# Optimization experiments

Hardware: AMD Instinct MI355X
Metric: run time of the kernel (lower is better)

The kernel has to match this reference:

```python
import jax, jax.numpy as jnp
from jax import lax
import numpy as np

ITER_ = 10
SMOOTH = 1.0

# ---------- soft skeletonization (clDice-style, 2D) ----------

def _max_pool(x, wh, ww):
    # x: [B,1,H,W]
    return lax.reduce_window(x, -jnp.inf, lax.max, (1, 1, wh, ww), (1, 1, 1, 1), 'SAME')

def _soft_erode(x):
    return jnp.minimum(-_max_pool(-x, 3, 1), -_max_pool(-x, 1, 3))

def _soft_dilate(x):
    return _max_pool(x, 3, 3)

def _soft_open(x):
    return _soft_dilate(_soft_erode(x))

def soft_skel(img, iters):
    skel = jax.nn.relu(img - _soft_open(img))
    for _ in range(iters):
        img = _soft_erode(img)
        delta = jax.nn.relu(img - _soft_open(img))
        skel = skel + jax.nn.relu(delta - skel * delta)
    return skel

# ---------- exact 2D Euclidean distance transform ----------

def _edt2d(mask):
    # mask: [H,W] bool, True = foreground. distance to nearest background pixel.
    H, W = mask.shape
    BIG = jnp.float32(H + W)
    z = ~mask  # background indicator
    def step(d, zr):
        d = jnp.where(zr, 0.0, jnp.minimum(d + 1.0, BIG))
        return d, d
    init = jnp.full((H,), BIG, jnp.float32)
    _, f = lax.scan(step, init, z.T)            # [W,H] forward along rows
    _, b = lax.scan(step, init, z.T[::-1])      # backward
    g = jnp.minimum(f, b[::-1]).T               # [H,W] 1D row distance
    ys = jnp.arange(H, dtype=jnp.float32)
    diff2 = (ys[:, None] - ys[None, :]) ** 2    # [H,H]
    # lower envelope over columns: d2[y,x] = min_y' g[y',x]^2 + (y-y')^2
    d2 = jnp.min(g[None, :, :] ** 2 + diff2[:, :, None], axis=1)  # [H,W]
    return jnp.sqrt(d2)

_edt_batched = jax.vmap(_edt2d)  # [B,H,W] bool -> [B,H,W] float

# ---------- cbDice pieces ----------

def combine_tensors(A, B, C):
    return jnp.where((A != 0) & (B == 0), A * C, B * C)

def get_weights(mask_input, skel_input, prob_flag):
    # mask_input/skel_input: [B,H,W] float
    mask = mask_input > 0.5
    skel = skel_input > 0.5
    dist = lax.stop_gradient(_edt_batched(mask))       # EDT of binary mask, non-diff
    distances = jnp.where(mask, dist, 0.0)
    skel_radius = jnp.where(skel, distances, 0.0)
    rmax = jnp.maximum(jnp.max(skel_radius, axis=(1, 2), keepdims=True), 1.0)
    rmin = jnp.maximum(jnp.min(skel_radius, axis=(1, 2), keepdims=True), 1.0)
    d_clip = jnp.minimum(distances, rmax)
    dist_map_norm = d_clip / rmax
    skel_R_norm = skel_radius / rmax
    I_norm = (rmax - skel_radius + rmin) / rmax        # dim == 2 branch
    I_norm = jnp.where(skel, I_norm, 0.0)
    if prob_flag:
        return dist_map_norm * mask_input, skel_R_norm * mask_input, I_norm * skel_input
    m = mask.astype(jnp.float32)
    s = skel.astype(jnp.float32)
    return dist_map_norm * m, skel_R_norm * m, I_norm * s

def soft_cb_dice_loss(y_pred, y_true):
    p = jax.nn.sigmoid(y_pred)                              # [B,1,H,W]
    pb = jnp.concatenate([1.0 - p, p], axis=1)              # [B,2,H,W]
    pp = jax.nn.softmax(pb, axis=1)[:, 1]                   # [B,H,W]
    yt = jnp.where(y_true > 0, 1.0, 0.0)[:, 0]              # [B,H,W]
    hard = lax.stop_gradient((pp > 0.5).astype(jnp.float32))
    skel_pred_hard = lax.stop_gradient(soft_skel(hard[:, None], ITER_)[:, 0])
    skel_true = lax.stop_gradient(soft_skel(yt[:, None], ITER_)[:, 0])
    skel_pred_prob = skel_pred_hard * pp
    q_vl, q_slvl, q_sl = get_weights(yt, skel_true, False)
    q_vp, q_spvp, q_sp = get_weights(pp, skel_pred_prob, True)
    w_tprec = (jnp.sum(q_sp * q_vl) + SMOOTH) / (jnp.sum(combine_tensors(q_spvp, q_slvl, q_sp)) + SMOOTH)
    w_tsens = (jnp.sum(q_sl * q_vp) + SMOOTH) / (jnp.sum(combine_tensors(q_slvl, q_spvp, q_sl)) + SMOOTH)
    return 1.0 - 2.0 * (w_tprec * w_tsens) / (w_tprec + w_tsens)

def setup_inputs() -> dict:
    key = jax.random.key(0)
    k1, k2 = jax.random.split(key)
    y_pred = jax.random.normal(k1, (4, 1, 256, 256), dtype=jnp.float32)
    y_true = jax.random.randint(k2, (4, 1, 256, 256), 0, 2, dtype=jnp.int32)
    return {"y_pred": y_pred, "y_true": y_true}

def reference(y_pred, y_true):
    return soft_cb_dice_loss(y_pred, y_true)
```

## Files before the change

### kernel.cpp

```cpp
#include <hip/hip_runtime.h>

typedef unsigned long long u64;

#define NIMG 4
#define H 256
#define W 256
#define NPIX (H*W)
#define NTOT (NIMG*NPIX)
#define WPR 4
#define WPI (H*WPR)
#define WPB (NIMG*WPI)
#define XT 16

__global__ void prep_kernel(const float* __restrict__ y_pred,
                            const int* __restrict__ y_true,
                            float* __restrict__ pp,
                            u64* __restrict__ mask_bits,
                            unsigned* __restrict__ rmm_u,
                            double* __restrict__ sums) {
  if (blockIdx.x == 0) {
    if (threadIdx.x < 16) rmm_u[threadIdx.x] = (threadIdx.x & 1) ? 0x7F800000u : 0u;
    else if (threadIdx.x < 20) sums[threadIdx.x - 16] = 0.0;
  }
  int i = blockIdx.x * 256 + threadIdx.x;
  float x = y_pred[i];
  float p = 1.0f / (1.0f + expf(-x));
  float q = 1.0f / (1.0f + expf(-(2.0f * p - 1.0f)));
  pp[i] = q;
  u64 bt = __ballot(y_true[i] > 0);
  u64 bp = __ballot(q > 0.5f);
  if ((threadIdx.x & 63) == 0) {
    mask_bits[i >> 6] = bt;
    mask_bits[WPB + (i >> 6)] = bp;
  }
}

__device__ __forceinline__ void erode_from(const u64 S[][WPR], int y, u64 out[WPR]) {
  u64 c[WPR], up[WPR], dn[WPR];
#pragma unroll
  for (int k = 0; k < WPR; ++k) {
    c[k]  = S[y][k];
    up[k] = (y > 0)     ? S[y-1][k] : ~0ULL;
    dn[k] = (y < H-1)   ? S[y+1][k] : ~0ULL;
  }
#pragma unroll
  for (int k = 0; k < WPR; ++k) {
    u64 l = (c[k] << 1) | ((k > 0)     ? (c[k-1] >> 63) : 1ULL);
    u64 r = (c[k] >> 1) | ((k < WPR-1) ? (c[k+1] << 63) : 0x8000000000000000ULL);
    out[k] = c[k] & up[k] & dn[k] & l & r;
  }
}

__device__ __forceinline__ void dilate_from(const u64 S[][WPR], int y, u64 out[WPR]) {
  u64 v[WPR];
#pragma unroll
  for (int k = 0; k < WPR; ++k) {
    u64 a = S[y][k];
    if (y > 0)   a |= S[y-1][k];
    if (y < H-1) a |= S[y+1][k];
    v[k] = a;
  }
#pragma unroll
  for (int k = 0; k < WPR; ++k) {
    u64 l = (v[k] << 1) | ((k > 0)     ? (v[k-1] >> 63) : 0ULL);
    u64 r = (v[k] >> 1) | ((k < WPR-1) ? (v[k+1] << 63) : 0ULL);
    out[k] = v[k] | l | r;
  }
}

__global__ void skel_kernel(const u64* __restrict__ mask_bits,
                            u64* __restrict__ skel_bits) {
  __shared__ u64 SA[H][WPR];
  __shared__ u64 SB[H][WPR];
  int y = threadIdx.x;
  int base = blockIdx.x * WPI;
  u64 a[WPR], cur[WPR], e[WPR], d[WPR], sk[WPR];
#pragma unroll
  for (int k = 0; k < WPR; ++k) { a[k] = mask_bits[base + y*WPR + k]; SA[y][k] = a[k]; }
  __syncthreads();
  erode_from(SA, y, e);
#pragma unroll
  for (int k = 0; k < WPR; ++k) SB[y][k] = e[k];
  __syncthreads();
  dilate_from(SB, y, d);
#pragma unroll
  for (int k = 0; k < WPR; ++k) { sk[k] = a[k] & ~d[k]; cur[k] = e[k]; }
  u64 (*P)[WPR] = SB;
  u64 (*Q)[WPR] = SA;
  for (int it = 0; it < 10; ++it) {
    erode_from(P, y, e);
#pragma unroll
    for (int k = 0; k < WPR; ++k) Q[y][k] = e[k];
    __syncthreads();
    dilate_from(Q, y, d);
#pragma unroll
    for (int k = 0; k < WPR; ++k) { sk[k] |= cur[k] & ~d[k]; cur[k] = e[k]; }
    u64 (*T)[WPR] = P; P = Q; Q = T;
  }
#pragma unroll
  for (int k = 0; k < WPR; ++k) skel_bits[base + y*WPR + k] = sk[k];
}

__global__ void edt_cols_kernel(const u64* __restrict__ mask_bits,
                                const u64* __restrict__ skel_bits,
                                float* __restrict__ edt,
                                unsigned* __restrict__ rmm_u) {
  __shared__ float col2[H][XT + 1];
  int bi = blockIdx.x >> 4;
  int xt = blockIdx.x & 15;
  int x0 = xt * XT;
  int kx = x0 >> 6;
  int sh0 = x0 & 63;
  int t = threadIdx.x;
  {
    int y = t;
    const u64* row = mask_bits + bi*WPI + y*WPR;
    u64 z[WPR];
#pragma unroll
    for (int k = 0; k < WPR; ++k) z[k] = ~row[k];
#pragma unroll
    for (int xx = 0; xx < XT; ++xx) {
      int x = x0 + xx;
      int bx = x & 63;
      int ld = 512;
      {
        u64 w = z[kx] & ((bx == 63) ? ~0ULL : ((1ULL << (bx+1)) - 1ULL));
        for (int k = kx; ; ) {
          if (w) { int pos = 63 - __builtin_clzll(w) + (k << 6); ld = x - pos; break; }
          if (--k < 0) break;
          w = z[k];
        }
      }
      int rd = 512;
      {
        u64 w = z[kx] & (~0ULL << bx);
        for (int k = kx; ; ) {
          if (w) { int pos = __builtin_ctzll(w) + (k << 6); rd = pos - x; break; }
          if (++k > WPR-1) break;
          w = z[k];
        }
      }
      int g = min(ld, rd);
      col2[y][xx] = (float)(g * g);
    }
  }
  __syncthreads();
  int x  = t & (XT - 1);
  int yg = t >> 4;
  float vmax = 0.0f, vmin = 3.0e38f;
#pragma unroll
  for (int j = 0; j < 16; ++j) {
    int y = yg * 16 + j;
    float best = col2[y][x];
    for (int k = 1; k < H; ++k) {
      float k2 = (float)(k * k);
      if (k2 >= best) break;
      int ym = y - k, yq = y + k;
      if (ym >= 0) best = fminf(best, col2[ym][x] + k2);
      if (yq < H)  best = fminf(best, col2[yq][x] + k2);
    }
    float dist = sqrtf(best);
    edt[bi*NPIX + y*W + x0 + x] = dist;
    u64 sw = skel_bits[bi*WPI + y*WPR + kx];
    int sb = (int)((sw >> (sh0 + x)) & 1ULL);
    float srad = sb ? dist : 0.0f;
    vmax = fmaxf(vmax, srad);
    vmin = fminf(vmin, srad);
  }
  for (int o = 32; o > 0; o >>= 1) {
    vmax = fmaxf(vmax, __shfl_down(vmax, o, 64));
    vmin = fminf(vmin, __shfl_down(vmin, o, 64));
  }
  __shared__ float smax[4], smin[4];
  int wave = t >> 6, lane = t & 63;
  if (lane == 0) { smax[wave] = vmax; smin[wave] = vmin; }
  __syncthreads();
  if (t == 0) {
    float mx = smax[0], mn = smin[0];
    for (int wv = 1; wv < 4; ++wv) { mx = fmaxf(mx, smax[wv]); mn = fminf(mn, smin[wv]); }
    atomicMax(&rmm_u[bi*2 + 0], __float_as_uint(mx));
    atomicMin(&rmm_u[bi*2 + 1], __float_as_uint(mn));
  }
}

__global__ void final_sum_kernel(const float* __restrict__ edt,
                                 const u64* __restrict__ mask_bits,
                                 const u64* __restrict__ skel_bits,
                                 const float* __restrict__ pp,
                                 const unsigned* __restrict__ rmm_u,
                                 double* __restrict__ sums) {
  int i0 = (blockIdx.x * 256 + threadIdx.x) * 4;
  int img = i0 >> 16;
  int wi = i0 >> 6;
  int b0 = i0 & 63;
  u64 mw_t = mask_bits[wi];
  u64 sw_t = skel_bits[wi];
  u64 sw_p = skel_bits[WPB + wi];
  float4 d_t4 = *(const float4*)(edt + i0);
  float4 d_p4 = *(const float4*)(edt + NTOT + i0);
  float4 pp4  = *(const float4*)(pp + i0);
  float rmax_t = fmaxf(__uint_as_float(rmm_u[img*2 + 0]), 1.0f);
  float rmin_t = fmaxf(__uint_as_float(rmm_u[img*2 + 1]), 1.0f);
  float rmax_p = fmaxf(__uint_as_float(rmm_u[(4+img)*2 + 0]), 1.0f);
  float rmin_p = fmaxf(__uint_as_float(rmm_u[(4+img)*2 + 1]), 1.0f);
  float t1 = 0.f, t2 = 0.f, t3 = 0.f, t4 = 0.f;
  float dts[4] = {d_t4.x, d_t4.y, d_t4.z, d_t4.w};
  float dps[4] = {d_p4.x, d_p4.y, d_p4.z, d_p4.w};
  float pps[4] = {pp4.x, pp4.y, pp4.z, pp4.w};
#pragma unroll
  for (int j = 0; j < 4; ++j) {
    int b = b0 + j;
    int m_t = (int)((mw_t >> b) & 1ULL);
    int s_t = (int)((sw_t >> b) & 1ULL);
    float distances_t = m_t ? dts[j] : 0.0f;
    float skelrad_t   = s_t ? distances_t : 0.0f;
    float dmn_t = fminf(distances_t, rmax_t) / rmax_t;
    float srn_t = skelrad_t / rmax_t;
    float In_t  = s_t ? (rmax_t - skelrad_t + rmin_t) / rmax_t : 0.0f;
    float q_vl   = m_t ? dmn_t : 0.0f;
    float q_slvl = m_t ? srn_t : 0.0f;
    float q_sl   = s_t ? In_t  : 0.0f;
    int s_pb = (int)((sw_p >> b) & 1ULL);
    float ppv = pps[j];
    float skel_in_p = s_pb ? ppv : 0.0f;
    bool msk_p = ppv > 0.5f;
    bool sk_p  = skel_in_p > 0.5f;
    float distances_p = msk_p ? dps[j] : 0.0f;
    float skelrad_p   = sk_p ? distances_p : 0.0f;
    float dmn_p = fminf(distances_p, rmax_p) / rmax_p;
    float srn_p = skelrad_p / rmax_p;
    float In_p  = sk_p ? (rmax_p - skelrad_p + rmin_p) / rmax_p : 0.0f;
    float q_vp   = dmn_p * ppv;
    float q_spvp = srn_p * ppv;
    float q_sp   = In_p * skel_in_p;
    t1 += q_sp * q_vl;
    t2 += (q_spvp != 0.0f && q_slvl == 0.0f) ? q_spvp * q_sp : q_slvl * q_sp;
    t3 += q_sl * q_vp;
    t4 += (q_slvl != 0.0f && q_spvp == 0.0f) ? q_slvl * q_sl : q_spvp * q_sl;
  }
  for (int o = 32; o > 0; o >>= 1) {
    t1 += __shfl_down(t1, o, 64);
    t2 += __shfl_down(t2, o, 64);
    t3 += __shfl_down(t3, o, 64);
    t4 += __shfl_down(t4, o, 64);
  }
  __shared__ float part[4][4];
  int wave = threadIdx.x >> 6, lane = threadIdx.x & 63;
  if (lane == 0) { part[wave][0]=t1; part[wave][1]=t2; part[wave][2]=t3; part[wave][3]=t4; }
  __syncthreads();
  if (threadIdx.x == 0) {
    float a0=0,a1=0,a2=0,a3=0;
    for (int wv = 0; wv < 4; ++wv) {
      a0 += part[wv][0]; a1 += part[wv][1]; a2 += part[wv][2]; a3 += part[wv][3];
    }
    atomicAdd(&sums[0], (double)a0);
    atomicAdd(&sums[1], (double)a1);
    atomicAdd(&sums[2], (double)a2);
    atomicAdd(&sums[3], (double)a3);
  }
}

__global__ void finalize_kernel(const double* __restrict__ sums,
                                float* __restrict__ out) {
  double wp  = (sums[0] + 1.0) / (sums[1] + 1.0);
  double wsn = (sums[2] + 1.0) / (sums[3] + 1.0);
  double loss = 1.0 - 2.0 * (wp * wsn) / (wp + wsn);
  out[0] = (float)loss;
}

extern "C" void kernel_launch(void* const* d_in, const int* in_sizes, int n_in,
                              void* d_out, int out_size, void* d_ws, size_t ws_size,
                              hipStream_t stream) {
  (void)in_sizes; (void)n_in; (void)out_size; (void)ws_size;
  const float* y_pred = (const float*)d_in[0];
  const int*   y_true = (const int*)d_in[1];
  float* out = (float*)d_out;
  char* ws = (char*)d_ws;

  float* pp        = (float*)(ws + 0);
  float* edt       = (float*)(ws + 1048576);
  u64*   mask_bits = (u64*)  (ws + 3145728);
  u64*   skel_bits = (u64*)  (ws + 3211264);
  unsigned* rmm_u  = (unsigned*)(ws + 3276800);
  double* sums     = (double*)(ws + 3276864);

  prep_kernel<<<NTOT/256, 256, 0, stream>>>(y_pred, y_true, pp, mask_bits, rmm_u, sums);
  skel_kernel<<<8, 256, 0, stream>>>(mask_bits, skel_bits);
  edt_cols_kernel<<<8*(W/XT), 256, 0, stream>>>(mask_bits, skel_bits, edt, rmm_u);
  final_sum_kernel<<<NTOT/1024, 256, 0, stream>>>(edt, mask_bits, skel_bits, pp, rmm_u, sums);
  finalize_kernel<<<1, 1, 0, stream>>>(sums, out);
}
```

Measured before the change: 96.19 us.

## Fuse skeletonization into EDT kernel and fold finalize into last-block reduction

Each EDT column-tile block now recomputes the 10-iteration bitwise skeleton for its image redundantly in shared memory, removing the separate 8-block skel kernel and its launch and serialization. The finalize kernel is folded into final_sum via an atomic completion counter, with the last block computing the loss. This trades 16x redundant skeleton work per image for two fewer launches and more parallel occupancy.

```diff
diff --git a/kernel.cpp b/kernel.cpp
--- a/kernel.cpp
+++ b/kernel.cpp
@@ -17,10 +17,12 @@
                             float* __restrict__ pp,
                             u64* __restrict__ mask_bits,
                             unsigned* __restrict__ rmm_u,
-                            double* __restrict__ sums) {
+                            double* __restrict__ sums,
+                            unsigned* __restrict__ count) {
   if (blockIdx.x == 0) {
     if (threadIdx.x < 16) rmm_u[threadIdx.x] = (threadIdx.x & 1) ? 0x7F800000u : 0u;
     else if (threadIdx.x < 20) sums[threadIdx.x - 16] = 0.0;
+    else if (threadIdx.x == 20) *count = 0u;
   }
   int i = blockIdx.x * 256 + threadIdx.x;
   float x = y_pred[i];
@@ -68,43 +70,12 @@
   }
 }
 
-__global__ void skel_kernel(const u64* __restrict__ mask_bits,
-                            u64* __restrict__ skel_bits) {
+__global__ void edt_skel_kernel(const u64* __restrict__ mask_bits,
+                                u64* __restrict__ skel_bits,
+                                float* __restrict__ edt,
+                                unsigned* __restrict__ rmm_u) {
   __shared__ u64 SA[H][WPR];
   __shared__ u64 SB[H][WPR];
-  int y = threadIdx.x;
-  int base = blockIdx.x * WPI;
-  u64 a[WPR], cur[WPR], e[WPR], d[WPR], sk[WPR];
-#pragma unroll
-  for (int k = 0; k < WPR; ++k) { a[k] = mask_bits[base + y*WPR + k]; SA[y][k] = a[k]; }
-  __syncthreads();
-  erode_from(SA, y, e);
-#pragma unroll
-  for (int k = 0; k < WPR; ++k) SB[y][k] = e[k];
-  __syncthreads();
-  dilate_from(SB, y, d);
-#pragma unroll
-  for (int k = 0; k < WPR; ++k) { sk[k] = a[k] & ~d[k]; cur[k] = e[k]; }
-  u64 (*P)[WPR] = SB;
-  u64 (*Q)[WPR] = SA;
-  for (int it = 0; it < 10; ++it) {
-    erode_from(P, y, e);
-#pragma unroll
-    for (int k = 0; k < WPR; ++k) Q[y][k] = e[k];
-    __syncthreads();
-    dilate_from(Q, y, d);
-#pragma unroll
-    for (int k = 0; k < WPR; ++k) { sk[k] |= cur[k] & ~d[k]; cur[k] = e[k]; }
-    u64 (*T)[WPR] = P; P = Q; Q = T;
-  }
-#pragma unroll
-  for (int k = 0; k < WPR; ++k) skel_bits[base + y*WPR + k] = sk[k];
-}
-
-__global__ void edt_cols_kernel(const u64* __restrict__ mask_bits,
-                                const u64* __restrict__ skel_bits,
-                                float* __restrict__ edt,
-                                unsigned* __restrict__ rmm_u) {
   __shared__ float col2[H][XT + 1];
   int bi = blockIdx.x >> 4;
   int xt = blockIdx.x & 15;
@@ -112,12 +83,15 @@
   int kx = x0 >> 6;
   int sh0 = x0 & 63;
   int t = threadIdx.x;
+  int y = t;
+  const u64* rowp = mask_bits + bi*WPI + y*WPR;
+  u64 a[WPR];
+#pragma unroll
+  for (int k = 0; k < WPR; ++k) a[k] = rowp[k];
   {
-    int y = t;
-    const u64* row = mask_bits + bi*WPI + y*WPR;
     u64 z[WPR];
 #pragma unroll
-    for (int k = 0; k < WPR; ++k) z[k] = ~row[k];
+    for (int k = 0; k < WPR; ++k) z[k] = ~a[k];
 #pragma unroll
     for (int xx = 0; xx < XT; ++xx) {
       int x = x0 + xx;
@@ -144,25 +118,54 @@
       col2[y][xx] = (float)(g * g);
     }
   }
+  u64 cur[WPR], e[WPR], d[WPR], sk[WPR];
+#pragma unroll
+  for (int k = 0; k < WPR; ++k) SA[y][k] = a[k];
+  __syncthreads();
+  erode_from(SA, y, e);
+#pragma unroll
+  for (int k = 0; k < WPR; ++k) SB[y][k] = e[k];
+  __syncthreads();
+  dilate_from(SB, y, d);
+#pragma unroll
+  for (int k = 0; k < WPR; ++k) { sk[k] = a[k] & ~d[k]; cur[k] = e[k]; }
+  u64 (*P)[WPR] = SB;
+  u64 (*Q)[WPR] = SA;
+  for (int it = 0; it < 10; ++it) {
+    erode_from(P, y, e);
+#pragma unroll
+    for (int k = 0; k < WPR; ++k) Q[y][k] = e[k];
+    __syncthreads();
+    dilate_from(Q, y, d);
+#pragma unroll
+    for (int k = 0; k < WPR; ++k) { sk[k] |= cur[k] & ~d[k]; cur[k] = e[k]; }
+    u64 (*T)[WPR] = P; P = Q; Q = T;
+  }
+  u64 (*SK)[WPR] = Q;
+#pragma unroll
+  for (int k = 0; k < WPR; ++k) SK[y][k] = sk[k];
+  if (xt == 0) {
+#pragma unroll
+    for (int k = 0; k < WPR; ++k) skel_bits[bi*WPI + y*WPR + k] = sk[k];
+  }
   __syncthreads();
   int x  = t & (XT - 1);
   int yg = t >> 4;
   float vmax = 0.0f, vmin = 3.0e38f;
 #pragma unroll
   for (int j = 0; j < 16; ++j) {
-    int y = yg * 16 + j;
-    float best = col2[y][x];
+    int yy = yg * 16 + j;
+    float best = col2[yy][x];
     for (int k = 1; k < H; ++k) {
       float k2 = (float)(k * k);
       if (k2 >= best) break;
-      int ym = y - k, yq = y + k;
+      int ym = yy - k, yq = yy + k;
       if (ym >= 0) best = fminf(best, col2[ym][x] + k2);
       if (yq < H)  best = fminf(best, col2[yq][x] + k2);
     }
     float dist = sqrtf(best);
-    edt[bi*NPIX + y*W + x0 + x] = dist;
-    u64 sw = skel_bits[bi*WPI + y*WPR + kx];
-    int sb = (int)((sw >> (sh0 + x)) & 1ULL);
+    edt[bi*NPIX + yy*W + x0 + x] = dist;
+    int sb = (int)((SK[yy][kx] >> (sh0 + x)) & 1ULL);
     float srad = sb ? dist : 0.0f;
     vmax = fmaxf(vmax, srad);
     vmin = fminf(vmin, srad);
@@ -188,7 +191,9 @@
                                  const u64* __restrict__ skel_bits,
                                  const float* __restrict__ pp,
                                  const unsigned* __restrict__ rmm_u,
-                                 double* __restrict__ sums) {
+                                 double* __restrict__ sums,
+                                 unsigned* __restrict__ count,
+                                 float* __restrict__ out) {
   int i0 = (blockIdx.x * 256 + threadIdx.x) * 4;
   int img = i0 >> 16;
   int wi = i0 >> 6;
@@ -253,19 +258,22 @@
     for (int wv = 0; wv < 4; ++wv) {
       a0 += part[wv][0]; a1 += part[wv][1]; a2 += part[wv][2]; a3 += part[wv][3];
     }
-    atomicAdd(&sums[0], (double)a0);
-    atomicAdd(&sums[1], (double)a1);
-    atomicAdd(&sums[2], (double)a2);
-    atomicAdd(&sums[3], (double)a3);
-  }
-}
-
-__global__ void finalize_kernel(const double* __restrict__ sums,
-                                float* __restrict__ out) {
-  double wp  = (sums[0] + 1.0) / (sums[1] + 1.0);
-  double wsn = (sums[2] + 1.0) / (sums[3] + 1.0);
-  double loss = 1.0 - 2.0 * (wp * wsn) / (wp + wsn);
-  out[0] = (float)loss;
+    double o0 = atomicAdd(&sums[0], (double)a0);
+    double o1 = atomicAdd(&sums[1], (double)a1);
+    double o2 = atomicAdd(&sums[2], (double)a2);
+    double o3 = atomicAdd(&sums[3], (double)a3);
+    asm volatile("" :: "v"(o0), "v"(o1), "v"(o2), "v"(o3) : "memory");
+    unsigned old = atomicAdd(count, 1u);
+    if (old == gridDim.x - 1) {
+      double s0 = atomicAdd(&sums[0], 0.0);
+      double s1 = atomicAdd(&sums[1], 0.0);
+      double s2 = atomicAdd(&sums[2], 0.0);
+      double s3 = atomicAdd(&sums[3], 0.0);
+      double wp  = (s0 + 1.0) / (s1 + 1.0);
+      double wsn = (s2 + 1.0) / (s3 + 1.0);
+      out[0] = (float)(1.0 - 2.0 * (wp * wsn) / (wp + wsn));
+    }
+  }
 }
 
 extern "C" void kernel_launch(void* const* d_in, const int* in_sizes, int n_in,
@@ -283,10 +291,9 @@
   u64*   skel_bits = (u64*)  (ws + 3211264);
   unsigned* rmm_u  = (unsigned*)(ws + 3276800);
   double* sums     = (double*)(ws + 3276864);
-
-  prep_kernel<<<NTOT/256, 256, 0, stream>>>(y_pred, y_true, pp, mask_bits, rmm_u, sums);
-  skel_kernel<<<8, 256, 0, stream>>>(mask_bits, skel_bits);
-  edt_cols_kernel<<<8*(W/XT), 256, 0, stream>>>(mask_bits, skel_bits, edt, rmm_u);
-  final_sum_kernel<<<NTOT/1024, 256, 0, stream>>>(edt, mask_bits, skel_bits, pp, rmm_u, sums);
-  finalize_kernel<<<1, 1, 0, stream>>>(sums, out);
-}
+  unsigned* count  = (unsigned*)(ws + 3276896);
+
+  prep_kernel<<<NTOT/256, 256, 0, stream>>>(y_pred, y_true, pp, mask_bits, rmm_u, sums, count);
+  edt_skel_kernel<<<8*(W/XT), 256, 0, stream>>>(mask_bits, skel_bits, edt, rmm_u);
+  final_sum_kernel<<<NTOT/1024, 256, 0, stream>>>(edt, mask_bits, skel_bits, pp, rmm_u, sums, count, out);
+}
```

Result: no change. 98.10 us (+2.0%).
